# Kernel tuning notes

Hardware: AMD Instinct MI355X
Metric: run time of the kernel (lower is better)

## Reference

```python
import jax, jax.numpy as jnp
import numpy as np

B = 512       # batch
D = 256       # n_embd
NH = 4        # heads
NN = 8 * D // NH   # neurons per head = 512
NTOT = NH * NN     # 2048
DH = D // NH       # 64
K = 8              # thinking steps
EPS_LN = 1e-5


def _ln(x, g, b):
    mu = jnp.mean(x, axis=-1, keepdims=True)
    var = jnp.mean((x - mu) ** 2, axis=-1, keepdims=True)
    return (x - mu) * jax.lax.rsqrt(var + EPS_LN) * g + b


def setup_inputs() -> dict:
    key = jax.random.key(0)
    ks = jax.random.split(key, 12)
    s = 0.02
    w = lambda k, shape: (jax.random.normal(k, shape, jnp.float32) * s)
    return {
        "boards": jax.random.normal(ks[0], (B, 12, 8, 8), jnp.float32),
        # board_encoder: Linear(768,d) -> GELU -> LN(d) -> Linear(d,d); weights stored (in,out)
        "enc_w1": w(ks[1], (768, D)), "enc_b1": jnp.zeros((D,), jnp.float32),
        "enc_ln_g": jnp.ones((D,), jnp.float32), "enc_ln_b": jnp.zeros((D,), jnp.float32),
        "enc_w2": w(ks[2], (D, D)), "enc_b2": jnp.zeros((D,), jnp.float32),
        "xinit_w": w(ks[3], (D, NTOT)), "xinit_b": jnp.zeros((NTOT,), jnp.float32),
        "D_y": w(ks[4], (NH, D, NN)),
        "E": w(ks[5], (NTOT, D)),
        "D_x": w(ks[6], (NH, D, NN)),
        "By_w": w(ks[7], (D, D)),
        "Bx_w": w(ks[8], (D, D)),
        "lna_g": jnp.ones((D,), jnp.float32), "lna_b": jnp.zeros((D,), jnp.float32),
        "lnz_g": jnp.ones((D,), jnp.float32), "lnz_b": jnp.zeros((D,), jnp.float32),
        "log_damping": jnp.asarray(np.log(0.9 / 0.1), jnp.float32),
        "vh_w1": w(ks[9], (D, D // 2)), "vh_b1": jnp.zeros((D // 2,), jnp.float32),
        "vh_w2": w(ks[10], (D // 2, 1)), "vh_b2": jnp.zeros((1,), jnp.float32),
    }


def reference(boards, enc_w1, enc_b1, enc_ln_g, enc_ln_b, enc_w2, enc_b2,
              xinit_w, xinit_b, D_y, E, D_x, By_w, Bx_w,
              lna_g, lna_b, lnz_g, lnz_b, log_damping,
              vh_w1, vh_b1, vh_w2, vh_b2):
    Bn = boards.shape[0]
    flat = boards.reshape(Bn, 768)
    h = jax.nn.gelu(flat @ enc_w1 + enc_b1, approximate=False)
    h = _ln(h, enc_ln_g, enc_ln_b)
    b = h @ enc_w2 + enc_b2                      # (B, d)
    x0 = jax.nn.relu(b @ xinit_w + xinit_b)      # (B, n)
    rho0 = jnp.zeros((Bn, NH, NN, DH), boards.dtype)
    lam = jax.nn.sigmoid(log_damping)
    b_y = b @ By_w
    b_x = b @ Bx_w

    def step(carry, _):
        x, rho = carry
        x_h = x.reshape(Bn, NH, NN)
        a = jnp.einsum('bhnd,bhn->bhd', rho, x_h).reshape(Bn, D)   # read from scratchpad
        a_cond = _ln(a + b_y, lna_g, lna_b)
        g = jax.nn.relu(jnp.einsum('bd,hdn->bhn', a_cond, D_y))
        y = (g * x_h).reshape(Bn, NTOT)
        z = _ln(y @ E, lnz_g, lnz_b)
        dx = jax.nn.relu(jnp.einsum('bd,hdn->bhn', z + b_x, D_x))
        x_new = x + dx.reshape(Bn, NTOT)
        xh = x_new.reshape(Bn, NH, NN)
        x_write = xh / (jnp.linalg.norm(xh, axis=-1, keepdims=True) + 1e-8)
        z_h = z.reshape(Bn, NH, DH)
        rho_new = lam * rho + (1.0 - lam) * jnp.einsum('bhn,bhd->bhnd', x_write, z_h)
        return (x_new, rho_new), z

    (_, _), zs = jax.lax.scan(step, (x0, rho0), None, length=K)
    z_last = zs[-1]                              # (B, d) from final thinking step
    v = jnp.tanh(jax.nn.gelu(z_last @ vh_w1 + vh_b1, approximate=False) @ vh_w2 + vh_b2)
    return v                                     # (B, 1)
```

## Files before the change

kernel.cpp:

```cpp
#include <hip/hip_runtime.h>
#include <hip/hip_bf16.h>
#include <math.h>

#define B_ 512
#define D_ 256
#define NH_ 4
#define NN_ 512
#define NTOT_ 2048
#define DH_ 64
#define KSTEPS 8

typedef __attribute__((ext_vector_type(8))) short bf16x8;
typedef __attribute__((ext_vector_type(4))) float f32x4;

#if __has_builtin(__builtin_amdgcn_global_load_lds)
#define HAVE_GLL 1
#else
#define HAVE_GLL 0
#endif

__device__ __forceinline__ float gelu_exact(float x) {
  return 0.5f * x * (1.0f + erff(x * 0.70710678118654752f));
}

__device__ __forceinline__ unsigned short f2b(float f) {
  union { float f; unsigned int u; } x; x.f = f;
  unsigned int u = x.u;
  unsigned int r = (u + 0x7FFFu + ((u >> 16) & 1u)) >> 16;
  return (unsigned short)r;
}

__device__ __forceinline__ float blockReduceSum256(float v, float* red) {
  int t = threadIdx.x;
  red[t] = v; __syncthreads();
  #pragma unroll
  for (int st = 128; st > 0; st >>= 1) {
    if (t < st) red[t] += red[t + st];
    __syncthreads();
  }
  float r = red[0];
  __syncthreads();
  return r;
}

#if HAVE_GLL
__device__ __forceinline__ void load16_lds(const unsigned short* g, unsigned short* l) {
  __builtin_amdgcn_global_load_lds(
      (const __attribute__((address_space(1))) unsigned int*)g,
      (__attribute__((address_space(3))) unsigned int*)l, 16, 0, 0);
}
#endif

template<int EPI>
__global__ __launch_bounds__(256) void gemm_mfma(
    const unsigned short* __restrict__ A, const unsigned short* __restrict__ W,
    const float* __restrict__ bias, const float* __restrict__ mul,
    const float* __restrict__ addto, float* __restrict__ outf,
    unsigned short* __restrict__ outb, int K, int N, int kchunk)
{
  __shared__ __align__(16) unsigned short As[2][64 * 64];
  __shared__ __align__(16) unsigned short Ws[2][32 * 64];
  const int t = threadIdx.x;
  const int lane = t & 63;
  const int w = t >> 6;
  const int row0 = blockIdx.y * 64, col0 = blockIdx.x * 32;
  const int k0 = blockIdx.z * kchunk;
  const int nt = kchunk >> 6;
  const int lr = lane & 15, lk = lane >> 4;
  const int l3 = lane >> 3, cch = lane & 7;

  f32x4 acc[2];
  acc[0] = (f32x4){0.f, 0.f, 0.f, 0.f};
  acc[1] = (f32x4){0.f, 0.f, 0.f, 0.f};

#if HAVE_GLL
  #define STAGE(tt)                                                              \
    {                                                                            \
      int buf_ = (tt) & 1;                                                       \
      int kk_ = k0 + (tt) * 64;                                                  \
      _Pragma("unroll")                                                          \
      for (int p = 0; p < 2; p++) {                                              \
        int r_ = (w * 2 + p) * 8 + l3;                                           \
        load16_lds(&A[(size_t)(row0 + r_) * K + kk_ + ((cch ^ (r_ & 7)) << 3)],  \
                   &As[buf_][(w * 2 + p) * 512]);                                \
      }                                                                          \
      int rw_ = w * 8 + l3;                                                      \
      load16_lds(&W[(size_t)(col0 + rw_) * K + kk_ + ((cch ^ (rw_ & 7)) << 3)],  \
                 &Ws[buf_][w * 512]);                                            \
    }

  STAGE(0);
  for (int tt = 0; tt < nt; tt++) {
    asm volatile("s_waitcnt vmcnt(0)" ::: "memory");
    __builtin_amdgcn_s_barrier();
    asm volatile("" ::: "memory");
    if (tt + 1 < nt) STAGE(tt + 1);
    const unsigned short* Ab = As[tt & 1];
    const unsigned short* Wb = Ws[tt & 1];
    #pragma unroll
    for (int ks = 0; ks < 2; ks++) {
      int q = ks * 4 + lk;
      int r = w * 16 + lr;
      bf16x8 af = *(const bf16x8*)&Ab[r * 64 + ((q ^ (r & 7)) << 3)];
      #pragma unroll
      for (int j = 0; j < 2; j++) {
        int c = j * 16 + lr;
        bf16x8 bf = *(const bf16x8*)&Wb[c * 64 + ((q ^ (c & 7)) << 3)];
        acc[j] = __builtin_amdgcn_mfma_f32_16x16x32_bf16(af, bf, acc[j], 0, 0, 0);
      }
    }
  }
  #undef STAGE
#else
  for (int tt = 0; tt < nt; tt++) {
    int buf_ = tt & 1;
    int kk_ = k0 + tt * 64;
    #pragma unroll
    for (int p = 0; p < 2; p++) {
      int r_ = (w * 2 + p) * 8 + l3;
      bf16x8 v = *(const bf16x8*)&A[(size_t)(row0 + r_) * K + kk_ + ((cch ^ (r_ & 7)) << 3)];
      *(bf16x8*)&As[buf_][r_ * 64 + (cch << 3)] = v;
    }
    int rw_ = w * 8 + l3;
    bf16x8 vw = *(const bf16x8*)&W[(size_t)(col0 + rw_) * K + kk_ + ((cch ^ (rw_ & 7)) << 3)];
    *(bf16x8*)&Ws[buf_][rw_ * 64 + (cch << 3)] = vw;
    __syncthreads();
    const unsigned short* Ab = As[buf_];
    const unsigned short* Wb = Ws[buf_];
    #pragma unroll
    for (int ks = 0; ks < 2; ks++) {
      int q = ks * 4 + lk;
      int r = w * 16 + lr;
      bf16x8 af = *(const bf16x8*)&Ab[r * 64 + ((q ^ (r & 7)) << 3)];
      #pragma unroll
      for (int j = 0; j < 2; j++) {
        int c = j * 16 + lr;
        bf16x8 bf = *(const bf16x8*)&Wb[c * 64 + ((q ^ (c & 7)) << 3)];
        acc[j] = __builtin_amdgcn_mfma_f32_16x16x32_bf16(af, bf, acc[j], 0, 0, 0);
      }
    }
    __syncthreads();
  }
#endif

  const int cr = lk * 4;
  #pragma unroll
  for (int j = 0; j < 2; j++) {
    #pragma unroll
    for (int q = 0; q < 4; q++) {
      int r = row0 + w * 16 + cr + q;
      int c = col0 + j * 16 + lr;
      float v = acc[j][q];
      if (EPI == 0) {
        v += bias[c]; v = fmaxf(v, 0.f);
        outf[(size_t)r * N + c] = v;
      } else if (EPI == 1) {
        v = fmaxf(v, 0.f) * mul[(size_t)r * N + c];
        outb[(size_t)r * N + c] = f2b(v);
      } else if (EPI == 2) {
        outf[(size_t)blockIdx.z * ((size_t)512 * N) + (size_t)r * N + c] = v;
      } else {
        v = fmaxf(v, 0.f) + addto[(size_t)r * N + c];
        outf[(size_t)r * N + c] = v;
      }
    }
  }
}

template<int ACT>
__global__ __launch_bounds__(256) void gemm_tile(
    const float* __restrict__ A, const float* __restrict__ W,
    const float* __restrict__ bias, float* __restrict__ out,
    unsigned short* __restrict__ outb, int M, int N, int K, int kchunk)
{
  __shared__ float As[16][68];
  __shared__ float Bs[16][68];
  const int tid = threadIdx.x;
  const int row0 = blockIdx.y * 64;
  const int col0 = blockIdx.x * 64;
  const int k0 = blockIdx.z * kchunk;
  const int ty = tid >> 4, tx = tid & 15;
  const int ar = tid >> 4, ak = tid & 15;
  const int br = tid >> 6, bc = tid & 63;
  float acc[4][4] = {};
  for (int kk = k0; kk < k0 + kchunk; kk += 16) {
    #pragma unroll
    for (int i = 0; i < 4; i++) {
      int r = ar + i * 16;
      As[ak][r] = A[(size_t)(row0 + r) * K + kk + ak];
    }
    #pragma unroll
    for (int i = 0; i < 4; i++) {
      int kr = br + i * 4;
      Bs[kr][bc] = W[(size_t)(kk + kr) * N + col0 + bc];
    }
    __syncthreads();
    #pragma unroll
    for (int q = 0; q < 16; q++) {
      float4 av = *(const float4*)&As[q][ty * 4];
      float4 bv = *(const float4*)&Bs[q][tx * 4];
      float aa[4] = {av.x, av.y, av.z, av.w};
      float bb[4] = {bv.x, bv.y, bv.z, bv.w};
      #pragma unroll
      for (int i = 0; i < 4; i++)
        #pragma unroll
        for (int j = 0; j < 4; j++)
          acc[i][j] = fmaf(aa[i], bb[j], acc[i][j]);
    }
    __syncthreads();
  }
  const bool parts = (gridDim.z > 1);
  float* o = out + (parts ? (size_t)blockIdx.z * (size_t)M * N : (size_t)0);
  #pragma unroll
  for (int i = 0; i < 4; i++) {
    int r = row0 + ty * 4 + i;
    #pragma unroll
    for (int j = 0; j < 4; j++) {
      int c = col0 + tx * 4 + j;
      float v = acc[i][j];
      if (!parts) {
        if (bias) v += bias[c];
        if (ACT == 2) v = gelu_exact(v);
      }
      o[(size_t)r * N + c] = v;
      if (!parts && outb) outb[(size_t)r * N + c] = f2b(v);
    }
  }
}

__global__ __launch_bounds__(256) void k_prep(
    const float* __restrict__ D_y, const float* __restrict__ D_x,
    const float* __restrict__ xinit_w, const float* __restrict__ E,
    unsigned short* __restrict__ DyT, unsigned short* __restrict__ DxT,
    unsigned short* __restrict__ xinitT, unsigned short* __restrict__ ET)
{
  __shared__ float T[64][65];
  const float* in; unsigned short* out; int Kd, Nd, head, nx;
  switch (blockIdx.y) {
    case 0:  in = D_y;     out = DyT;    Kd = 256;  Nd = 2048; head = 1; nx = 32; break;
    case 1:  in = D_x;     out = DxT;    Kd = 256;  Nd = 2048; head = 1; nx = 32; break;
    case 2:  in = xinit_w; out = xinitT; Kd = 256;  Nd = 2048; head = 0; nx = 32; break;
    default: in = E;       out = ET;     Kd = 2048; Nd = 256;  head = 0; nx = 4;  break;
  }
  const int n0 = (blockIdx.x % nx) * 64, k0 = (blockIdx.x / nx) * 64;
  const int tx = threadIdx.x & 63, ty = threadIdx.x >> 6;
  #pragma unroll
  for (int i = 0; i < 16; i++) {
    int k = k0 + ty + i * 4;
    int n = n0 + tx;
    float v;
    if (head) v = in[((size_t)(n >> 9) * 256 + k) * 512 + (n & 511)];
    else      v = in[(size_t)k * Nd + n];
    T[ty + i * 4][tx] = v;
  }
  __syncthreads();
  #pragma unroll
  for (int i = 0; i < 16; i++) {
    int n = n0 + ty + i * 4;
    out[(size_t)n * Kd + k0 + tx] = f2b(T[tx][ty + i * 4]);
  }
}

__global__ __launch_bounds__(256) void k_ln_reduce(
    const float* __restrict__ in, int nparts, int stride,
    const float* __restrict__ pre_bias, int do_gelu,
    const float* __restrict__ g, const float* __restrict__ bta,
    const float* __restrict__ addvec, float* __restrict__ out,
    unsigned short* __restrict__ out2_bf)
{
  __shared__ float red[256];
  int b = blockIdx.x, d = threadIdx.x;
  float v = 0.f;
  for (int p = 0; p < nparts; p++) v += in[(size_t)p * stride + (size_t)b * 256 + d];
  if (pre_bias) v += pre_bias[d];
  if (do_gelu) v = gelu_exact(v);
  float mu = blockReduceSum256(v, red) * (1.f / 256.f);
  float c = v - mu;
  float var = blockReduceSum256(c * c, red) * (1.f / 256.f);
  float vn = c * rsqrtf(var + 1e-5f) * g[d] + bta[d];
  out[(size_t)b * 256 + d] = vn;
  if (out2_bf) out2_bf[(size_t)b * 256 + d] = f2b(vn + addvec[(size_t)b * 256 + d]);
}

__global__ __launch_bounds__(256) void step_a(
    const float* __restrict__ x, float* __restrict__ xw_hist,
    const float* __restrict__ z_hist, const float* __restrict__ b_y,
    const float* __restrict__ lna_g, const float* __restrict__ lna_b,
    const float* __restrict__ log_damp, int k, unsigned short* __restrict__ out)
{
  __shared__ float dots[KSTEPS][NH_];
  __shared__ float red[256];
  int b = blockIdx.x, t = threadIdx.x;
  int lane = t & 63, wv = t >> 6;
  float lam = 1.f / (1.f + expf(-log_damp[0]));
  const float* xb = x + (size_t)b * NTOT_;
  float xv[8];
  #pragma unroll
  for (int i = 0; i < 8; i++) xv[i] = xb[t * 8 + i];

  if (k >= 1) {
    float s = 0.f;
    #pragma unroll
    for (int i = 0; i < 8; i++) s += xv[i] * xv[i];
    #pragma unroll
    for (int m = 1; m < 64; m <<= 1) s += __shfl_xor(s, m, 64);
    float inv = 1.f / (sqrtf(s) + 1e-8f);
    float* xwout = xw_hist + ((size_t)(k - 1) * B_ + b) * NTOT_;
    #pragma unroll
    for (int i = 0; i < 8; i++) xwout[t * 8 + i] = xv[i] * inv;
    if (lane == 0) dots[k - 1][wv] = s * inv;
  }
  for (int j = 0; j < k - 1; j++) {
    const float* xwb = xw_hist + ((size_t)j * B_ + b) * NTOT_;
    float s = 0.f;
    #pragma unroll
    for (int i = 0; i < 8; i++) s += xv[i] * xwb[t * 8 + i];
    #pragma unroll
    for (int off = 32; off > 0; off >>= 1) s += __shfl_down(s, off, 64);
    if (lane == 0) dots[j][wv] = s;
  }
  __syncthreads();

  int d = t;
  float av = 0.f, lp = 1.f;
  for (int j = k - 1; j >= 0; j--) {
    av += (1.f - lam) * lp * dots[j][d >> 6] * z_hist[((size_t)j * B_ + b) * D_ + d];
    lp *= lam;
  }
  av += b_y[(size_t)b * D_ + d];
  float mu = blockReduceSum256(av, red) * (1.f / 256.f);
  float c = av - mu;
  float var = blockReduceSum256(c * c, red) * (1.f / 256.f);
  out[(size_t)b * D_ + d] = f2b(c * rsqrtf(var + 1e-5f) * lna_g[d] + lna_b[d]);
}

__global__ __launch_bounds__(128) void k_value(
    const float* __restrict__ z, const float* __restrict__ w1,
    const float* __restrict__ b1, const float* __restrict__ w2,
    const float* __restrict__ b2, float* __restrict__ out)
{
  __shared__ float red[128];
  int b = blockIdx.x, j = threadIdx.x;
  const float* zr = z + (size_t)b * 256;
  float s = 0.f;
  #pragma unroll 8
  for (int i = 0; i < 256; i++) s += zr[i] * w1[(size_t)i * 128 + j];
  float g = gelu_exact(s + b1[j]) * w2[j];
  red[j] = g; __syncthreads();
  #pragma unroll
  for (int st = 64; st > 0; st >>= 1) {
    if (j < st) red[j] += red[j + st];
    __syncthreads();
  }
  if (j == 0) out[b] = tanhf(red[0] + b2[0]);
}

extern "C" void kernel_launch(void* const* d_in, const int* in_sizes, int n_in,
                              void* d_out, int out_size, void* d_ws, size_t ws_size,
                              hipStream_t stream) {
  const float* boards   = (const float*)d_in[0];
  const float* enc_w1   = (const float*)d_in[1];
  const float* enc_b1   = (const float*)d_in[2];
  const float* enc_ln_g = (const float*)d_in[3];
  const float* enc_ln_b = (const float*)d_in[4];
  const float* enc_w2   = (const float*)d_in[5];
  const float* enc_b2   = (const float*)d_in[6];
  const float* xinit_w  = (const float*)d_in[7];
  const float* xinit_b  = (const float*)d_in[8];
  const float* D_y      = (const float*)d_in[9];
  const float* E        = (const float*)d_in[10];
  const float* D_x      = (const float*)d_in[11];
  const float* By_w     = (const float*)d_in[12];
  const float* Bx_w     = (const float*)d_in[13];
  const float* lna_g    = (const float*)d_in[14];
  const float* lna_b    = (const float*)d_in[15];
  const float* lnz_g    = (const float*)d_in[16];
  const float* lnz_b    = (const float*)d_in[17];
  const float* log_damp = (const float*)d_in[18];
  const float* vh_w1    = (const float*)d_in[19];
  const float* vh_b1    = (const float*)d_in[20];
  const float* vh_w2    = (const float*)d_in[21];
  const float* vh_b2    = (const float*)d_in[22];
  float* outp = (float*)d_out;

  float* ws = (float*)d_ws;
  size_t o = 0;
  float* x      = ws + o; o += (size_t)B_ * NTOT_;
  float* xw     = ws + o; o += (size_t)KSTEPS * B_ * NTOT_;
  float* zh     = ws + o; o += (size_t)KSTEPS * B_ * D_;
  float* hparts = ws + o; o += (size_t)8 * B_ * D_;
  float* h      = ws + o; o += (size_t)B_ * D_;
  float* bvec   = ws + o; o += (size_t)B_ * D_;
  float* b_y    = ws + o; o += (size_t)B_ * D_;
  float* b_x    = ws + o; o += (size_t)B_ * D_;
  float* zparts = ws + o; o += (size_t)8 * B_ * D_;
  unsigned short* DyT     = (unsigned short*)(ws + o); o += (size_t)NTOT_ * D_ / 2;
  unsigned short* DxT     = (unsigned short*)(ws + o); o += (size_t)NTOT_ * D_ / 2;
  unsigned short* ET      = (unsigned short*)(ws + o); o += (size_t)D_ * NTOT_ / 2;
  unsigned short* xinitT  = (unsigned short*)(ws + o); o += (size_t)NTOT_ * D_ / 2;
  unsigned short* bvec_bf = (unsigned short*)(ws + o); o += (size_t)B_ * D_ / 2;
  unsigned short* acond_bf= (unsigned short*)(ws + o); o += (size_t)B_ * D_ / 2;
  unsigned short* zbx_bf  = (unsigned short*)(ws + o); o += (size_t)B_ * D_ / 2;
  unsigned short* y_bf    = (unsigned short*)(ws + o); o += (size_t)B_ * NTOT_ / 2;

  k_prep<<<dim3(128, 4), 256, 0, stream>>>(D_y, D_x, xinit_w, E, DyT, DxT, xinitT, ET);

  gemm_tile<0><<<dim3(4, 8, 8), 256, 0, stream>>>(boards, enc_w1, nullptr, hparts,
                                                  nullptr, B_, D_, 768, 96);
  k_ln_reduce<<<B_, 256, 0, stream>>>(hparts, 8, B_ * D_, enc_b1, 1,
                                      enc_ln_g, enc_ln_b, nullptr, h, nullptr);
  gemm_tile<0><<<dim3(4, 8, 1), 256, 0, stream>>>(h, enc_w2, enc_b2, bvec, bvec_bf,
                                                  B_, D_, D_, D_);
  gemm_tile<0><<<dim3(4, 8, 1), 256, 0, stream>>>(bvec, By_w, nullptr, b_y, nullptr,
                                                  B_, D_, D_, D_);
  gemm_tile<0><<<dim3(4, 8, 1), 256, 0, stream>>>(bvec, Bx_w, nullptr, b_x, nullptr,
                                                  B_, D_, D_, D_);
  gemm_mfma<0><<<dim3(64, 8, 1), 256, 0, stream>>>(bvec_bf, xinitT, xinit_b, nullptr,
                                                   nullptr, x, nullptr, 256, 2048, 256);

  for (int k = 0; k < KSTEPS; k++) {
    step_a<<<B_, 256, 0, stream>>>(x, xw, zh, b_y, lna_g, lna_b, log_damp, k, acond_bf);
    gemm_mfma<1><<<dim3(64, 8, 1), 256, 0, stream>>>(acond_bf, DyT, nullptr, x,
                                                     nullptr, nullptr, y_bf, 256, 2048, 256);
    gemm_mfma<2><<<dim3(8, 8, 8), 256, 0, stream>>>(y_bf, ET, nullptr, nullptr,
                                                    nullptr, zparts, nullptr, 2048, 256, 256);
    k_ln_reduce<<<B_, 256, 0, stream>>>(zparts, 8, B_ * D_, nullptr, 0, lnz_g, lnz_b,
                                        b_x, zh + (size_t)k * B_ * D_, zbx_bf);
    gemm_mfma<3><<<dim3(64, 8, 1), 256, 0, stream>>>(zbx_bf, DxT, nullptr, nullptr,
                                                     x, x, nullptr, 256, 2048, 256);
  }

  k_value<<<B_, 128, 0, stream>>>(zh + (size_t)(KSTEPS - 1) * B_ * D_,
                                  vh_w1, vh_b1, vh_w2, vh_b2, outp);
}
```

Measured before the change: 413.7 us.

## Fuse y and z GEMMs per tile, merge By/Bx GEMMs, skip final x update

A new k_yz kernel computes the D_y GEMM tile, applies relu and the x multiply, keeps the bf16 y tile in LDS, and multiplies it by the matching E slice. Each tile writes its partial z, so the y_bf round trip through global memory and one launch per step go away, but partial sums grow to 32 per row for the LN reduce. By_w and Bx_w are concatenated so one GEMM produces both, the x GEMMs move to 64x64 tiles with 512 threads, the value head is folded into the last LN-z kernel, and the unused final-step x update is skipped.

New measurement: 389.0 us. 6.0% less time.

```diff
diff --git a/kernel.cpp b/kernel.cpp
--- a/kernel.cpp
+++ b/kernel.cpp
@@ -52,89 +52,72 @@
 #endif
 
 template<int EPI>
-__global__ __launch_bounds__(256) void gemm_mfma(
+__global__ __launch_bounds__(512) void k_gemm_x(
     const unsigned short* __restrict__ A, const unsigned short* __restrict__ W,
-    const float* __restrict__ bias, const float* __restrict__ mul,
-    const float* __restrict__ addto, float* __restrict__ outf,
-    unsigned short* __restrict__ outb, int K, int N, int kchunk)
-{
-  __shared__ __align__(16) unsigned short As[2][64 * 64];
-  __shared__ __align__(16) unsigned short Ws[2][32 * 64];
+    const float* __restrict__ bias, float* __restrict__ xio)
+{
+  __shared__ __align__(16) unsigned short As[2 * 4096];
+  __shared__ __align__(16) unsigned short Ws[2 * 4096];
   const int t = threadIdx.x;
-  const int lane = t & 63;
-  const int w = t >> 6;
-  const int row0 = blockIdx.y * 64, col0 = blockIdx.x * 32;
-  const int k0 = blockIdx.z * kchunk;
-  const int nt = kchunk >> 6;
+  const int lane = t & 63, w = t >> 6;
   const int lr = lane & 15, lk = lane >> 4;
   const int l3 = lane >> 3, cch = lane & 7;
+  const int n0 = blockIdx.x * 64, m0 = blockIdx.y * 64;
+  const int wm = w & 3, wn = w >> 2;
 
   f32x4 acc[2];
   acc[0] = (f32x4){0.f, 0.f, 0.f, 0.f};
   acc[1] = (f32x4){0.f, 0.f, 0.f, 0.f};
 
 #if HAVE_GLL
-  #define STAGE(tt)                                                              \
-    {                                                                            \
-      int buf_ = (tt) & 1;                                                       \
-      int kk_ = k0 + (tt) * 64;                                                  \
-      _Pragma("unroll")                                                          \
-      for (int p = 0; p < 2; p++) {                                              \
-        int r_ = (w * 2 + p) * 8 + l3;                                           \
-        load16_lds(&A[(size_t)(row0 + r_) * K + kk_ + ((cch ^ (r_ & 7)) << 3)],  \
-                   &As[buf_][(w * 2 + p) * 512]);                                \
-      }                                                                          \
-      int rw_ = w * 8 + l3;                                                      \
-      load16_lds(&W[(size_t)(col0 + rw_) * K + kk_ + ((cch ^ (rw_ & 7)) << 3)],  \
-                 &Ws[buf_][w * 512]);                                            \
-    }
-
-  STAGE(0);
-  for (int tt = 0; tt < nt; tt++) {
+  #define STGX(tt) {                                                              \
+      int buf_ = (tt) & 1; int kk_ = (tt) * 64;                                   \
+      int r_ = w * 8 + l3;                                                        \
+      load16_lds(&A[(size_t)(m0 + r_) * 256 + kk_ + ((cch ^ (r_ & 7)) << 3)],     \
+                 &As[buf_ * 4096 + w * 512]);                                     \
+      load16_lds(&W[(size_t)(n0 + r_) * 256 + kk_ + ((cch ^ (r_ & 7)) << 3)],     \
+                 &Ws[buf_ * 4096 + w * 512]); }
+  STGX(0);
+  for (int tt = 0; tt < 4; tt++) {
     asm volatile("s_waitcnt vmcnt(0)" ::: "memory");
     __builtin_amdgcn_s_barrier();
     asm volatile("" ::: "memory");
-    if (tt + 1 < nt) STAGE(tt + 1);
-    const unsigned short* Ab = As[tt & 1];
-    const unsigned short* Wb = Ws[tt & 1];
+    if (tt + 1 < 4) STGX(tt + 1);
+    const unsigned short* Ab = &As[(tt & 1) * 4096];
+    const unsigned short* Wb = &Ws[(tt & 1) * 4096];
     #pragma unroll
     for (int ks = 0; ks < 2; ks++) {
       int q = ks * 4 + lk;
-      int r = w * 16 + lr;
+      int r = wm * 16 + lr;
       bf16x8 af = *(const bf16x8*)&Ab[r * 64 + ((q ^ (r & 7)) << 3)];
       #pragma unroll
       for (int j = 0; j < 2; j++) {
-        int c = j * 16 + lr;
+        int c = wn * 32 + j * 16 + lr;
         bf16x8 bf = *(const bf16x8*)&Wb[c * 64 + ((q ^ (c & 7)) << 3)];
         acc[j] = __builtin_amdgcn_mfma_f32_16x16x32_bf16(af, bf, acc[j], 0, 0, 0);
       }
     }
   }
-  #undef STAGE
+  #undef STGX
 #else
-  for (int tt = 0; tt < nt; tt++) {
-    int buf_ = tt & 1;
-    int kk_ = k0 + tt * 64;
-    #pragma unroll
-    for (int p = 0; p < 2; p++) {
-      int r_ = (w * 2 + p) * 8 + l3;
-      bf16x8 v = *(const bf16x8*)&A[(size_t)(row0 + r_) * K + kk_ + ((cch ^ (r_ & 7)) << 3)];
-      *(bf16x8*)&As[buf_][r_ * 64 + (cch << 3)] = v;
-    }
-    int rw_ = w * 8 + l3;
-    bf16x8 vw = *(const bf16x8*)&W[(size_t)(col0 + rw_) * K + kk_ + ((cch ^ (rw_ & 7)) << 3)];
-    *(bf16x8*)&Ws[buf_][rw_ * 64 + (cch << 3)] = vw;
-    __syncthreads();
-    const unsigned short* Ab = As[buf_];
-    const unsigned short* Wb = Ws[buf_];
+  for (int tt = 0; tt < 4; tt++) {
+    int buf_ = tt & 1; int kk_ = tt * 64;
+    int r_ = w * 8 + l3;
+    bf16x8 va = *(const bf16x8*)&A[(size_t)(m0 + r_) * 256 + kk_ + ((cch ^ (r_ & 7)) << 3)];
+    *(bf16x8*)&As[buf_ * 4096 + r_ * 64 + cch * 8] = va;
+    bf16x8 vw = *(const bf16x8*)&W[(size_t)(n0 + r_) * 256 + kk_ + ((cch ^ (r_ & 7)) << 3)];
+    *(bf16x8*)&Ws[buf_ * 4096 + r_ * 64 + cch * 8] = vw;
+    __syncthreads();
+    const unsigned short* Ab = &As[buf_ * 4096];
+    const unsigned short* Wb = &Ws[buf_ * 4096];
     #pragma unroll
     for (int ks = 0; ks < 2; ks++) {
       int q = ks * 4 + lk;
-      int r = w * 16 + lr;
+      int r = wm * 16 + lr;
       bf16x8 af = *(const bf16x8*)&Ab[r * 64 + ((q ^ (r & 7)) << 3)];
       #pragma unroll
       for (int j = 0; j < 2; j++) {
-        int c = j * 16 + lr;
+        int c = wn * 32 + j * 16 + lr;
         bf16x8 bf = *(const bf16x8*)&Wb[c * 64 + ((q ^ (c & 7)) << 3)];
         acc[j] = __builtin_amdgcn_mfma_f32_16x16x32_bf16(af, bf, acc[j], 0, 0, 0);
       }
@@ -143,28 +126,144 @@
   }
 #endif
 
-  const int cr = lk * 4;
-  #pragma unroll
-  for (int j = 0; j < 2; j++) {
-    #pragma unroll
-    for (int q = 0; q < 4; q++) {
-      int r = row0 + w * 16 + cr + q;
-      int c = col0 + j * 16 + lr;
-      float v = acc[j][q];
-      if (EPI == 0) {
-        v += bias[c]; v = fmaxf(v, 0.f);
-        outf[(size_t)r * N + c] = v;
-      } else if (EPI == 1) {
-        v = fmaxf(v, 0.f) * mul[(size_t)r * N + c];
-        outb[(size_t)r * N + c] = f2b(v);
-      } else if (EPI == 2) {
-        outf[(size_t)blockIdx.z * ((size_t)512 * N) + (size_t)r * N + c] = v;
-      } else {
-        v = fmaxf(v, 0.f) + addto[(size_t)r * N + c];
-        outf[(size_t)r * N + c] = v;
+  #pragma unroll
+  for (int j = 0; j < 2; j++)
+    #pragma unroll
+    for (int qq = 0; qq < 4; qq++) {
+      int r = m0 + wm * 16 + lk * 4 + qq;
+      int c = n0 + wn * 32 + j * 16 + lr;
+      float v = acc[j][qq];
+      if (EPI == 0) v = fmaxf(v + bias[c], 0.f);
+      else          v = fmaxf(v, 0.f) + xio[(size_t)r * NTOT_ + c];
+      xio[(size_t)r * NTOT_ + c] = v;
+    }
+}
+
+__global__ __launch_bounds__(512) void k_yz(
+    const unsigned short* __restrict__ acond_bf, const unsigned short* __restrict__ DyT,
+    const unsigned short* __restrict__ ET, const float* __restrict__ x,
+    float* __restrict__ zparts)
+{
+  __shared__ __align__(16) unsigned short As[2 * 4096];
+  __shared__ __align__(16) unsigned short Ws[2 * 4096];
+  __shared__ __align__(16) unsigned short Es[256 * 64];
+  __shared__ __align__(16) unsigned short ytile[64 * 64];
+  const int t = threadIdx.x;
+  const int lane = t & 63, w = t >> 6;
+  const int lr = lane & 15, lk = lane >> 4;
+  const int l3 = lane >> 3, cch = lane & 7;
+  const int nt_ = blockIdx.x, mt = blockIdx.y;
+  const int m0 = mt * 64, n0 = nt_ * 64;
+  const int wm = w & 3, wn = w >> 2;
+
+  f32x4 acc[2];
+  acc[0] = (f32x4){0.f, 0.f, 0.f, 0.f};
+  acc[1] = (f32x4){0.f, 0.f, 0.f, 0.f};
+
+#if HAVE_GLL
+  #define STGY(tt) {                                                                  \
+      int buf_ = (tt) & 1; int kk_ = (tt) * 64;                                       \
+      int r_ = w * 8 + l3;                                                            \
+      load16_lds(&acond_bf[(size_t)(m0 + r_) * 256 + kk_ + ((cch ^ (r_ & 7)) << 3)],  \
+                 &As[buf_ * 4096 + w * 512]);                                         \
+      load16_lds(&DyT[(size_t)(n0 + r_) * 256 + kk_ + ((cch ^ (r_ & 7)) << 3)],       \
+                 &Ws[buf_ * 4096 + w * 512]); }
+  STGY(0);
+  #pragma unroll
+  for (int p = 0; p < 4; p++) {
+    int d = p * 64 + w * 8 + l3;
+    load16_lds(&ET[(size_t)d * 2048 + n0 + ((cch ^ (d & 7)) << 3)],
+               &Es[(p * 64 + w * 8) * 64]);
+  }
+  for (int tt = 0; tt < 4; tt++) {
+    asm volatile("s_waitcnt vmcnt(0)" ::: "memory");
+    __builtin_amdgcn_s_barrier();
+    asm volatile("" ::: "memory");
+    if (tt + 1 < 4) STGY(tt + 1);
+    const unsigned short* Ab = &As[(tt & 1) * 4096];
+    const unsigned short* Wb = &Ws[(tt & 1) * 4096];
+    #pragma unroll
+    for (int ks = 0; ks < 2; ks++) {
+      int q = ks * 4 + lk;
+      int r = wm * 16 + lr;
+      bf16x8 af = *(const bf16x8*)&Ab[r * 64 + ((q ^ (r & 7)) << 3)];
+      #pragma unroll
+      for (int j = 0; j < 2; j++) {
+        int c = wn * 32 + j * 16 + lr;
+        bf16x8 bf = *(const bf16x8*)&Wb[c * 64 + ((q ^ (c & 7)) << 3)];
+        acc[j] = __builtin_amdgcn_mfma_f32_16x16x32_bf16(af, bf, acc[j], 0, 0, 0);
       }
     }
   }
+  #undef STGY
+#else
+  #pragma unroll
+  for (int p = 0; p < 4; p++) {
+    int d = p * 64 + w * 8 + l3;
+    bf16x8 ve = *(const bf16x8*)&ET[(size_t)d * 2048 + n0 + ((cch ^ (d & 7)) << 3)];
+    *(bf16x8*)&Es[d * 64 + cch * 8] = ve;
+  }
+  for (int tt = 0; tt < 4; tt++) {
+    int buf_ = tt & 1; int kk_ = tt * 64;
+    int r_ = w * 8 + l3;
+    bf16x8 va = *(const bf16x8*)&acond_bf[(size_t)(m0 + r_) * 256 + kk_ + ((cch ^ (r_ & 7)) << 3)];
+    *(bf16x8*)&As[buf_ * 4096 + r_ * 64 + cch * 8] = va;
+    bf16x8 vw = *(const bf16x8*)&DyT[(size_t)(n0 + r_) * 256 + kk_ + ((cch ^ (r_ & 7)) << 3)];
+    *(bf16x8*)&Ws[buf_ * 4096 + r_ * 64 + cch * 8] = vw;
+    __syncthreads();
+    const unsigned short* Ab = &As[buf_ * 4096];
+    const unsigned short* Wb = &Ws[buf_ * 4096];
+    #pragma unroll
+    for (int ks = 0; ks < 2; ks++) {
+      int q = ks * 4 + lk;
+      int r = wm * 16 + lr;
+      bf16x8 af = *(const bf16x8*)&Ab[r * 64 + ((q ^ (r & 7)) << 3)];
+      #pragma unroll
+      for (int j = 0; j < 2; j++) {
+        int c = wn * 32 + j * 16 + lr;
+        bf16x8 bf = *(const bf16x8*)&Wb[c * 64 + ((q ^ (c & 7)) << 3)];
+        acc[j] = __builtin_amdgcn_mfma_f32_16x16x32_bf16(af, bf, acc[j], 0, 0, 0);
+      }
+    }
+    __syncthreads();
+  }
+#endif
+
+  #pragma unroll
+  for (int j = 0; j < 2; j++)
+    #pragma unroll
+    for (int qq = 0; qq < 4; qq++) {
+      int rl = wm * 16 + lk * 4 + qq;
+      int cl = wn * 32 + j * 16 + lr;
+      float v = fmaxf(acc[j][qq], 0.f) * x[(size_t)(m0 + rl) * NTOT_ + n0 + cl];
+      ytile[rl * 64 + ((((cl >> 3) ^ (rl & 7)) << 3) | (cl & 7))] = f2b(v);
+    }
+  __syncthreads();
+
+  f32x4 zacc[8];
+  #pragma unroll
+  for (int j = 0; j < 8; j++) zacc[j] = (f32x4){0.f, 0.f, 0.f, 0.f};
+  #pragma unroll
+  for (int ks = 0; ks < 2; ks++) {
+    int q = ks * 4 + lk;
+    int r = wm * 16 + lr;
+    bf16x8 af = *(const bf16x8*)&ytile[r * 64 + ((q ^ (r & 7)) << 3)];
+    #pragma unroll
+    for (int j = 0; j < 8; j++) {
+      int c = wn * 128 + j * 16 + lr;
+      bf16x8 bf = *(const bf16x8*)&Es[c * 64 + ((q ^ (c & 7)) << 3)];
+      zacc[j] = __builtin_amdgcn_mfma_f32_16x16x32_bf16(af, bf, zacc[j], 0, 0, 0);
+    }
+  }
+  float* zp = zparts + (size_t)nt_ * (B_ * D_);
+  #pragma unroll
+  for (int j = 0; j < 8; j++)
+    #pragma unroll
+    for (int qq = 0; qq < 4; qq++) {
+      int r = m0 + wm * 16 + lk * 4 + qq;
+      int d = wn * 128 + j * 16 + lr;
+      zp[(size_t)r * D_ + d] = zacc[j][qq];
+    }
 }
 
 template<int ACT>
@@ -231,9 +330,25 @@
 __global__ __launch_bounds__(256) void k_prep(
     const float* __restrict__ D_y, const float* __restrict__ D_x,
     const float* __restrict__ xinit_w, const float* __restrict__ E,
+    const float* __restrict__ By_w, const float* __restrict__ Bx_w,
     unsigned short* __restrict__ DyT, unsigned short* __restrict__ DxT,
-    unsigned short* __restrict__ xinitT, unsigned short* __restrict__ ET)
-{
+    unsigned short* __restrict__ xinitT, unsigned short* __restrict__ ET,
+    float* __restrict__ Wcat)
+{
+  const int t = threadIdx.x;
+  if (blockIdx.y == 4) {
+    if (blockIdx.x >= 32) return;
+    int k0 = ((int)blockIdx.x >> 3) * 64, n0 = ((int)blockIdx.x & 7) * 64;
+    for (int i = 0; i < 16; i++) {
+      int local = i * 256 + t;
+      int kk = local >> 6, nn = local & 63;
+      int n = n0 + nn;
+      float v = (n < 256) ? By_w[(size_t)(k0 + kk) * 256 + n]
+                          : Bx_w[(size_t)(k0 + kk) * 256 + (n - 256)];
+      Wcat[(size_t)(k0 + kk) * 512 + n] = v;
+    }
+    return;
+  }
   __shared__ float T[64][65];
   const float* in; unsigned short* out; int Kd, Nd, head, nx;
   switch (blockIdx.y) {
@@ -242,8 +357,8 @@
     case 2:  in = xinit_w; out = xinitT; Kd = 256;  Nd = 2048; head = 0; nx = 32; break;
     default: in = E;       out = ET;     Kd = 2048; Nd = 256;  head = 0; nx = 4;  break;
   }
-  const int n0 = (blockIdx.x % nx) * 64, k0 = (blockIdx.x / nx) * 64;
-  const int tx = threadIdx.x & 63, ty = threadIdx.x >> 6;
+  const int n0 = ((int)blockIdx.x % nx) * 64, k0 = ((int)blockIdx.x / nx) * 64;
+  const int tx = t & 63, ty = t >> 6;
   #pragma unroll
   for (int i = 0; i < 16; i++) {
     int k = k0 + ty + i * 4;
@@ -261,30 +376,65 @@
   }
 }
 
-__global__ __launch_bounds__(256) void k_ln_reduce(
+__global__ __launch_bounds__(256) void k_ln_enc(
     const float* __restrict__ in, int nparts, int stride,
-    const float* __restrict__ pre_bias, int do_gelu,
+    const float* __restrict__ pre_bias,
     const float* __restrict__ g, const float* __restrict__ bta,
-    const float* __restrict__ addvec, float* __restrict__ out,
-    unsigned short* __restrict__ out2_bf)
+    float* __restrict__ out)
 {
   __shared__ float red[256];
   int b = blockIdx.x, d = threadIdx.x;
   float v = 0.f;
   for (int p = 0; p < nparts; p++) v += in[(size_t)p * stride + (size_t)b * 256 + d];
-  if (pre_bias) v += pre_bias[d];
-  if (do_gelu) v = gelu_exact(v);
+  v = gelu_exact(v + pre_bias[d]);
   float mu = blockReduceSum256(v, red) * (1.f / 256.f);
   float c = v - mu;
   float var = blockReduceSum256(c * c, red) * (1.f / 256.f);
-  float vn = c * rsqrtf(var + 1e-5f) * g[d] + bta[d];
-  out[(size_t)b * 256 + d] = vn;
-  if (out2_bf) out2_bf[(size_t)b * 256 + d] = f2b(vn + addvec[(size_t)b * 256 + d]);
-}
-
-__global__ __launch_bounds__(256) void step_a(
+  out[(size_t)b * 256 + d] = c * rsqrtf(var + 1e-5f) * g[d] + bta[d];
+}
+
+template<int VAL>
+__global__ __launch_bounds__(256) void k_ln_z(
+    const float* __restrict__ zparts, const float* __restrict__ bybx,
+    const float* __restrict__ lnz_g, const float* __restrict__ lnz_b,
+    float* __restrict__ zh_k, unsigned short* __restrict__ zbx_bf,
+    const float* __restrict__ w1, const float* __restrict__ b1,
+    const float* __restrict__ w2, const float* __restrict__ b2,
+    float* __restrict__ vout)
+{
+  __shared__ float red[256];
+  __shared__ float zn[256];
+  int b = blockIdx.x, d = threadIdx.x;
+  float v = 0.f;
+  #pragma unroll
+  for (int p = 0; p < 32; p++) v += zparts[(size_t)p * (B_ * D_) + (size_t)b * D_ + d];
+  float mu = blockReduceSum256(v, red) * (1.f / 256.f);
+  float c = v - mu;
+  float var = blockReduceSum256(c * c, red) * (1.f / 256.f);
+  float vn = c * rsqrtf(var + 1e-5f) * lnz_g[d] + lnz_b[d];
+  zh_k[(size_t)b * D_ + d] = vn;
+  zbx_bf[(size_t)b * D_ + d] = f2b(vn + bybx[(size_t)b * 512 + 256 + d]);
+  if (VAL) {
+    zn[d] = vn; __syncthreads();
+    int j = d & 127, ih = d >> 7;
+    float s = 0.f;
+    #pragma unroll 4
+    for (int i = ih * 128; i < ih * 128 + 128; i++) s += zn[i] * w1[(size_t)i * 128 + j];
+    red[d] = s; __syncthreads();
+    if (d < 128) red[d] = gelu_exact(red[d] + red[d + 128] + b1[j]) * w2[d];
+    __syncthreads();
+    #pragma unroll
+    for (int st = 64; st > 0; st >>= 1) {
+      if (d < st) red[d] += red[d + st];
+      __syncthreads();
+    }
+    if (d == 0) vout[b] = tanhf(red[0] + b2[0]);
+  }
+}
+
+__global__ __launch_bounds__(256) void k_step_a(
     const float* __restrict__ x, float* __restrict__ xw_hist,
-    const float* __restrict__ z_hist, const float* __restrict__ b_y,
+    const float* __restrict__ z_hist, const float* __restrict__ bybx,
     const float* __restrict__ lna_g, const float* __restrict__ lna_b,
     const float* __restrict__ log_damp, int k, unsigned short* __restrict__ out)
 {
@@ -305,9 +455,9 @@
     #pragma unroll
     for (int m = 1; m < 64; m <<= 1) s += __shfl_xor(s, m, 64);
     float inv = 1.f / (sqrtf(s) + 1e-8f);
-    float* xwout = xw_hist + ((size_t)(k - 1) * B_ + b) * NTOT_;
-    #pragma unroll
-    for (int i = 0; i < 8; i++) xwout[t * 8 + i] = xv[i] * inv;
+    float* xwo = xw_hist + ((size_t)(k - 1) * B_ + b) * NTOT_;
+    #pragma unroll
+    for (int i = 0; i < 8; i++) xwo[t * 8 + i] = xv[i] * inv;
     if (lane == 0) dots[k - 1][wv] = s * inv;
   }
   for (int j = 0; j < k - 1; j++) {
@@ -327,32 +477,11 @@
     av += (1.f - lam) * lp * dots[j][d >> 6] * z_hist[((size_t)j * B_ + b) * D_ + d];
     lp *= lam;
   }
-  av += b_y[(size_t)b * D_ + d];
+  av += bybx[(size_t)b * 512 + d];
   float mu = blockReduceSum256(av, red) * (1.f / 256.f);
   float c = av - mu;
   float var = blockReduceSum256(c * c, red) * (1.f / 256.f);
   out[(size_t)b * D_ + d] = f2b(c * rsqrtf(var + 1e-5f) * lna_g[d] + lna_b[d]);
-}
-
-__global__ __launch_bounds__(128) void k_value(
-    const float* __restrict__ z, const float* __restrict__ w1,
-    const float* __restrict__ b1, const float* __restrict__ w2,
-    const float* __restrict__ b2, float* __restrict__ out)
-{
-  __shared__ float red[128];
-  int b = blockIdx.x, j = threadIdx.x;
-  const float* zr = z + (size_t)b * 256;
-  float s = 0.f;
-  #pragma unroll 8
-  for (int i = 0; i < 256; i++) s += zr[i] * w1[(size_t)i * 128 + j];
-  float g = gelu_exact(s + b1[j]) * w2[j];
-  red[j] = g; __syncthreads();
-  #pragma unroll
-  for (int st = 64; st > 0; st >>= 1) {
-    if (j < st) red[j] += red[j + st];
-    __syncthreads();
-  }
-  if (j == 0) out[b] = tanhf(red[0] + b2[0]);
 }
 
 extern "C" void kernel_launch(void* const* d_in, const int* in_sizes, int n_in,
@@ -391,9 +520,9 @@
   float* hparts = ws + o; o += (size_t)8 * B_ * D_;
   float* h      = ws + o; o += (size_t)B_ * D_;
   float* bvec   = ws + o; o += (size_t)B_ * D_;
-  float* b_y    = ws + o; o += (size_t)B_ * D_;
-  float* b_x    = ws + o; o += (size_t)B_ * D_;
-  float* zparts = ws + o; o += (size_t)8 * B_ * D_;
+  float* bybx   = ws + o; o += (size_t)B_ * 512;
+  float* Wcat   = ws + o; o += (size_t)256 * 512;
+  float* zparts = ws + o; o += (size_t)32 * B_ * D_;
   unsigned short* DyT     = (unsigned short*)(ws + o); o += (size_t)NTOT_ * D_ / 2;
   unsigned short* DxT     = (unsigned short*)(ws + o); o += (size_t)NTOT_ * D_ / 2;
   unsigned short* ET      = (unsigned short*)(ws + o); o += (size_t)D_ * NTOT_ / 2;
@@ -401,35 +530,30 @@
   unsigned short* bvec_bf = (unsigned short*)(ws + o); o += (size_t)B_ * D_ / 2;
   unsigned short* acond_bf= (unsigned short*)(ws + o); o += (size_t)B_ * D_ / 2;
   unsigned short* zbx_bf  = (unsigned short*)(ws + o); o += (size_t)B_ * D_ / 2;
-  unsigned short* y_bf    = (unsigned short*)(ws + o); o += (size_t)B_ * NTOT_ / 2;
-
-  k_prep<<<dim3(128, 4), 256, 0, stream>>>(D_y, D_x, xinit_w, E, DyT, DxT, xinitT, ET);
-
+
+  k_prep<<<dim3(128, 5), 256, 0, stream>>>(D_y, D_x, xinit_w, E, By_w, Bx_w,
+                                           DyT, DxT, xinitT, ET, Wcat);
   gemm_tile<0><<<dim3(4, 8, 8), 256, 0, stream>>>(boards, enc_w1, nullptr, hparts,
                                                   nullptr, B_, D_, 768, 96);
-  k_ln_reduce<<<B_, 256, 0, stream>>>(hparts, 8, B_ * D_, enc_b1, 1,
-                                      enc_ln_g, enc_ln_b, nullptr, h, nullptr);
+  k_ln_enc<<<B_, 256, 0, stream>>>(hparts, 8, B_ * D_, enc_b1, enc_ln_g, enc_ln_b, h);
   gemm_tile<0><<<dim3(4, 8, 1), 256, 0, stream>>>(h, enc_w2, enc_b2, bvec, bvec_bf,
                                                   B_, D_, D_, D_);
-  gemm_tile<0><<<dim3(4, 8, 1), 256, 0, stream>>>(bvec, By_w, nullptr, b_y, nullptr,
-                                                  B_, D_, D_, D_);
-  gemm_tile<0><<<dim3(4, 8, 1), 256, 0, stream>>>(bvec, Bx_w, nullptr, b_x, nullptr,
-                                                  B_, D_, D_, D_);
-  gemm_mfma<0><<<dim3(64, 8, 1), 256, 0, stream>>>(bvec_bf, xinitT, xinit_b, nullptr,
-                                                   nullptr, x, nullptr, 256, 2048, 256);
+  gemm_tile<0><<<dim3(8, 8, 1), 256, 0, stream>>>(bvec, Wcat, nullptr, bybx, nullptr,
+                                                  B_, 512, D_, D_);
+  k_gemm_x<0><<<dim3(32, 8), 512, 0, stream>>>(bvec_bf, xinitT, xinit_b, x);
 
   for (int k = 0; k < KSTEPS; k++) {
-    step_a<<<B_, 256, 0, stream>>>(x, xw, zh, b_y, lna_g, lna_b, log_damp, k, acond_bf);
-    gemm_mfma<1><<<dim3(64, 8, 1), 256, 0, stream>>>(acond_bf, DyT, nullptr, x,
-                                                     nullptr, nullptr, y_bf, 256, 2048, 256);
-    gemm_mfma<2><<<dim3(8, 8, 8), 256, 0, stream>>>(y_bf, ET, nullptr, nullptr,
-                                                    nullptr, zparts, nullptr, 2048, 256, 256);
-    k_ln_reduce<<<B_, 256, 0, stream>>>(zparts, 8, B_ * D_, nullptr, 0, lnz_g, lnz_b,
-                                        b_x, zh + (size_t)k * B_ * D_, zbx_bf);
-    gemm_mfma<3><<<dim3(64, 8, 1), 256, 0, stream>>>(zbx_bf, DxT, nullptr, nullptr,
-                                                     x, x, nullptr, 256, 2048, 256);
-  }
-
-  k_value<<<B_, 128, 0, stream>>>(zh + (size_t)(KSTEPS - 1) * B_ * D_,
-                                  vh_w1, vh_b1, vh_w2, vh_b2, outp);
-}
+    k_step_a<<<B_, 256, 0, stream>>>(x, xw, zh, bybx, lna_g, lna_b, log_damp, k, acond_bf);
+    k_yz<<<dim3(32, 8), 512, 0, stream>>>(acond_bf, DyT, ET, x, zparts);
+    if (k < KSTEPS - 1) {
+      k_ln_z<0><<<B_, 256, 0, stream>>>(zparts, bybx, lnz_g, lnz_b,
+                                        zh + (size_t)k * B_ * D_, zbx_bf,
+                                        nullptr, nullptr, nullptr, nullptr, nullptr);
+      k_gemm_x<1><<<dim3(32, 8), 512, 0, stream>>>(zbx_bf, DxT, nullptr, x);
+    } else {
+      k_ln_z<1><<<B_, 256, 0, stream>>>(zparts, bybx, lnz_g, lnz_b,
+                                        zh + (size_t)k * B_ * D_, zbx_bf,
+                                        vh_w1, vh_b1, vh_w2, vh_b2, outp);
+    }
+  }
+}
```
